# Kernel optimization log

Hardware: AMD Instinct MI355X
Metric: run time of the kernel (lower is better)

The kernel has to match this reference:

```python
import jax, jax.numpy as jnp
import numpy as np
from jax import lax

B, T, H, F, K, NB, MAXLEN = 32, 1024, 384, 384, 3, 256, 2048


def _ln(x, g, b, eps=1e-5):
    m = jnp.mean(x, axis=-1, keepdims=True)
    v = jnp.var(x, axis=-1, keepdims=True)
    return (x - m) * lax.rsqrt(v + eps) * g + b


def _conv(x, w, b):
    # x: (B, T, Cin), w: (K, Cin, Cout); SAME padding == torch padding=(K-1)//2 for K=3, stride 1
    y = lax.conv_general_dilated(x, w, (1,), 'SAME', dimension_numbers=('NWC', 'WIO', 'NWC'))
    return y + b


def _predictor(x, mask, w1, b1, g1, be1, w2, b2, g2, be2, wo, bo):
    h = _ln(jax.nn.relu(_conv(x, w1, b1)), g1, be1)
    h = _ln(jax.nn.relu(_conv(h, w2, b2)), g2, be2)
    out = jnp.einsum('btf,f->bt', h, wo) + bo  # Linear(F -> 1).squeeze(-1)
    return jnp.where(mask, 0.0, out)


def _length_regulate(x, dur, max_len):
    # vectorized equivalent of torch per-sample expand+cat+pad
    csum = jnp.cumsum(dur, axis=1)                      # (B, T)
    total = csum[:, -1]                                 # (B,) = mel_len
    frames = jnp.arange(max_len)                        # (M,)
    # frame f belongs to phoneme i with csum[i-1] <= f < csum[i]
    idx = jax.vmap(lambda c: jnp.searchsorted(c, frames, side='right'))(csum)  # (B, M)
    idx = jnp.clip(idx, 0, x.shape[1] - 1)
    out = jnp.take_along_axis(x, idx[:, :, None], axis=1)                      # (B, M, H)
    valid = (frames[None, :] < total[:, None]).astype(x.dtype)                 # zero-pad tail
    return out * valid[:, :, None], total


def setup_inputs() -> dict:
    key = jax.random.key(0)
    ks = iter(jax.random.split(key, 64))
    nk = lambda: next(ks)
    d = {}
    d['x'] = jax.random.normal(nk(), (B, T, H), jnp.float32)
    d['src_mask'] = jnp.zeros((B, T), jnp.bool_)
    d['duration'] = jax.random.randint(nk(), (B, T), 0, 4)
    d['max_len'] = MAXLEN
    for p in ('dp', 'pp', 'ep'):
        d[p + '_w1'] = jax.random.normal(nk(), (K, H, F), jnp.float32) * 0.02
        d[p + '_b1'] = jnp.zeros((F,), jnp.float32)
        d[p + '_g1'] = jnp.ones((F,), jnp.float32)
        d[p + '_be1'] = jnp.zeros((F,), jnp.float32)
        d[p + '_w2'] = jax.random.normal(nk(), (K, F, F), jnp.float32) * 0.02
        d[p + '_b2'] = jnp.zeros((F,), jnp.float32)
        d[p + '_g2'] = jnp.ones((F,), jnp.float32)
        d[p + '_be2'] = jnp.zeros((F,), jnp.float32)
        d[p + '_wo'] = jax.random.normal(nk(), (F,), jnp.float32) * 0.02
        d[p + '_bo'] = jnp.zeros((1,), jnp.float32)
    d['pitch_bins'] = jnp.linspace(0.0, 1.0, NB - 1, dtype=jnp.float32)
    d['energy_bins'] = jnp.linspace(0.0, 1.0, NB - 1, dtype=jnp.float32)
    d['pitch_emb'] = jax.random.normal(nk(), (NB, H), jnp.float32) * 0.02
    d['energy_emb'] = jax.random.normal(nk(), (NB, H), jnp.float32) * 0.02
    d['pitch_target'] = jax.random.uniform(nk(), (B, T), jnp.float32)
    d['energy_target'] = jax.random.uniform(nk(), (B, T), jnp.float32)
    return d


def reference(x, src_mask, duration, max_len,
              dp_w1, dp_b1, dp_g1, dp_be1, dp_w2, dp_b2, dp_g2, dp_be2, dp_wo, dp_bo,
              pp_w1, pp_b1, pp_g1, pp_be1, pp_w2, pp_b2, pp_g2, pp_be2, pp_wo, pp_bo,
              ep_w1, ep_b1, ep_g1, ep_be1, ep_w2, ep_b2, ep_g2, ep_be2, ep_wo, ep_bo,
              pitch_bins, energy_bins, pitch_emb, energy_emb, pitch_target, energy_target):
    log_dur = _predictor(x, src_mask, dp_w1, dp_b1, dp_g1, dp_be1, dp_w2, dp_b2, dp_g2, dp_be2, dp_wo, dp_bo)
    # phoneme-level pitch (target path: bucketize target, torch.bucketize right=False == searchsorted left)
    pitch_pred = _predictor(x, src_mask, pp_w1, pp_b1, pp_g1, pp_be1, pp_w2, pp_b2, pp_g2, pp_be2, pp_wo, pp_bo)
    x = x + pitch_emb[jnp.searchsorted(pitch_bins, pitch_target, side='left')]
    # phoneme-level energy (predictor sees x AFTER pitch embedding add, as in torch)
    energy_pred = _predictor(x, src_mask, ep_w1, ep_b1, ep_g1, ep_be1, ep_w2, ep_b2, ep_g2, ep_be2, ep_wo, ep_bo)
    x = x + energy_emb[jnp.searchsorted(energy_bins, energy_target, side='left')]
    x_out, mel_len = _length_regulate(x, duration, max_len)
    return (x_out, pitch_pred, energy_pred, log_dur, mel_len)
```

## Files before the change

### kernel.cpp

```cpp
#include <hip/hip_runtime.h>

#define B_ 32
#define T_ 1024
#define C_ 384
#define MAXLEN_ 2048
#define NBINS_ 255
#define WPK1 442368
#define ARS 392
#define AROWS 82

typedef __attribute__((ext_vector_type(8))) short short8v;
typedef __attribute__((ext_vector_type(4))) float floatx4;

__device__ __forceinline__ unsigned short f2bf(float f) {
    unsigned u = __float_as_uint(f);
    u += 0x7fffu + ((u >> 16) & 1u);
    return (unsigned short)(u >> 16);
}

struct CvP {
    const float* xf;
    const unsigned short* wpk;
    const float* b1[3];  const float* g1[3];  const float* be1[3];
    const float* b2[3];  const float* g2[3];  const float* be2[3];
    const float* wo[3];  const float* bo[3];
    float* pred[3];
    const float* pbins; const float* pemb; const float* ptgt;
};

__global__ __launch_bounds__(512, 3) void conv_fused3(CvP P)
{
    __shared__ unsigned short As[AROWS * ARS];
    float* redS  = (float*)&As[68 * ARS];
    float* redQ  = redS + 640;
    float* prbuf = redQ + 640;
    int*   embi  = (int*)(prbuf + 512);

    const int tid  = threadIdx.x;
    const int wave = tid >> 6;
    const int lane = tid & 63;
    const int lq   = lane >> 4;
    const int ln   = lane & 15;
    const int p    = blockIdx.x >> 9;
    const int bi   = blockIdx.x & 511;
    const int b    = bi >> 4;
    const int t0   = (bi & 15) << 6;
    const int nb   = wave * 48;

    const unsigned short* b1base =
        P.wpk + (size_t)p * WPK1 + (size_t)(wave * 1536) + (size_t)lane * 8;
    short8v bA[3], bB[3];
#pragma unroll
    for (int nt = 0; nt < 3; ++nt) {
        bA[nt] = *(const short8v*)(b1base + (nt << 9));
        bB[nt] = *(const short8v*)(b1base + 12288 + (nt << 9));
    }

    const bool fuse_emb = (p == 2);
    if (fuse_emb) {
        if (tid < 68) {
            const int t = t0 - 2 + tid;
            int lo = 0;
            if ((unsigned)t < (unsigned)T_) {
                const float tg = P.ptgt[(b << 10) + t];
                int hi = NBINS_;
                while (lo < hi) {
                    const int mid = (lo + hi) >> 1;
                    if (P.pbins[mid] < tg) lo = mid + 1; else hi = mid;
                }
            }
            embi[tid] = lo;
        }
        __syncthreads();
    }
    for (int i = tid; i < 68 * 96; i += 512) {
        const int row = i / 96;
        const int c4  = i - row * 96;
        const int t   = t0 - 2 + row;
        uint2 pv = make_uint2(0u, 0u);
        if ((unsigned)t < (unsigned)T_) {
            float4 f = *(const float4*)(P.xf + ((size_t)(b << 10) + t) * C_ + c4 * 4);
            if (fuse_emb) {
                const float* er = P.pemb + (size_t)embi[row] * C_ + c4 * 4;
                f.x += er[0]; f.y += er[1]; f.z += er[2]; f.w += er[3];
            }
            asm("v_cvt_pk_bf16_f32 %0, %1, %2" : "=v"(pv.x) : "v"(f.x), "v"(f.y));
            asm("v_cvt_pk_bf16_f32 %0, %1, %2" : "=v"(pv.y) : "v"(f.z), "v"(f.w));
        }
        *(uint2*)&As[row * ARS + c4 * 4] = pv;
    }
    __syncthreads();

    floatx4 acc1[15];
#pragma unroll
    for (int i = 0; i < 15; ++i) acc1[i] = (floatx4){0.f, 0.f, 0.f, 0.f};

    const unsigned short* abase = &As[ln * ARS + lq * 8];
    {
        const unsigned short* bpA = b1base + 2 * 12288;
        const unsigned short* bpB = b1base + 3 * 12288;
#pragma unroll
        for (int kc = 0; kc < 3; ++kc) {
#pragma unroll
            for (int h2 = 0; h2 < 6; ++h2) {
                const int hb = h2 * 64;
                const int r  = kc * 12 + h2 * 2;
                {
                    short8v afrag[5];
#pragma unroll
                    for (int mt = 0; mt < 5; ++mt)
                        afrag[mt] = *(const short8v*)(abase + (mt * 16 + kc) * ARS + hb);
#pragma unroll
                    for (int mt = 0; mt < 5; ++mt)
#pragma unroll
                        for (int nt = 0; nt < 3; ++nt)
                            acc1[mt * 3 + nt] = __builtin_amdgcn_mfma_f32_16x16x32_bf16(
                                afrag[mt], bA[nt], acc1[mt * 3 + nt], 0, 0, 0);
                    if (r + 2 < 36) {
#pragma unroll
                        for (int nt = 0; nt < 3; ++nt)
                            bA[nt] = *(const short8v*)(bpA + (nt << 9));
                        bpA += 24576;
                    }
                }
                {
                    short8v afrag[5];
#pragma unroll
                    for (int mt = 0; mt < 5; ++mt)
                        afrag[mt] = *(const short8v*)(abase + (mt * 16 + kc) * ARS + hb + 32);
#pragma unroll
                    for (int mt = 0; mt < 5; ++mt)
#pragma unroll
                        for (int nt = 0; nt < 3; ++nt)
                            acc1[mt * 3 + nt] = __builtin_amdgcn_mfma_f32_16x16x32_bf16(
                                afrag[mt], bB[nt], acc1[mt * 3 + nt], 0, 0, 0);
                    if (r + 3 < 36) {
#pragma unroll
                        for (int nt = 0; nt < 3; ++nt)
                            bB[nt] = *(const short8v*)(bpB + (nt << 9));
                        bpB += 24576;
                    }
                }
            }
        }
    }
    __syncthreads();

    float c1b[3], c1g[3], c1be[3];
#pragma unroll
    for (int nt = 0; nt < 3; ++nt) {
        const int col = nb + nt * 16 + ln;
        c1b[nt]  = P.b1[p][col];
        c1g[nt]  = P.g1[p][col];
        c1be[nt] = P.be1[p][col];
    }
#pragma unroll
    for (int mt = 0; mt < 5; ++mt) {
#pragma unroll
        for (int rg = 0; rg < 4; ++rg) {
            float s = 0.f, q = 0.f;
#pragma unroll
            for (int nt = 0; nt < 3; ++nt) {
                float v = acc1[mt * 3 + nt][rg] + c1b[nt];
                v = v > 0.f ? v : 0.f;
                acc1[mt * 3 + nt][rg] = v;
                s += v; q += v * v;
            }
#pragma unroll
            for (int off = 1; off < 16; off <<= 1) {
                s += __shfl_xor(s, off, 64);
                q += __shfl_xor(q, off, 64);
            }
            if (ln == ((mt * 4 + rg) & 15)) {
                redS[wave * 80 + mt * 16 + lq * 4 + rg] = s;
                redQ[wave * 80 + mt * 16 + lq * 4 + rg] = q;
            }
        }
    }
    __syncthreads();

#pragma unroll
    for (int mt = 0; mt < 5; ++mt) {
#pragma unroll
        for (int rg = 0; rg < 4; ++rg) {
            const int j = mt * 16 + lq * 4 + rg;
            if (j < 66) {
                const int th = t0 - 1 + j;
                float s = 0.f, q = 0.f;
#pragma unroll
                for (int w = 0; w < 8; ++w) {
                    s += redS[w * 80 + j];
                    q += redQ[w * 80 + j];
                }
                const float m  = s * (1.f / 384.f);
                const float rs = rsqrtf(q * (1.f / 384.f) - m * m + 1e-5f);
                const bool valid = (unsigned)th < (unsigned)T_;
#pragma unroll
                for (int nt = 0; nt < 3; ++nt) {
                    float v = (acc1[mt * 3 + nt][rg] - m) * rs * c1g[nt] + c1be[nt];
                    if (!valid) v = 0.f;
                    As[j * ARS + nb + nt * 16 + ln] = f2bf(v);
                }
            }
        }
    }

    const unsigned short* b2base =
        P.wpk + (size_t)(3 + p) * WPK1 + (size_t)(wave * 1536) + (size_t)lane * 8;
#pragma unroll
    for (int nt = 0; nt < 3; ++nt) {
        bA[nt] = *(const short8v*)(b2base + (nt << 9));
        bB[nt] = *(const short8v*)(b2base + 12288 + (nt << 9));
    }
    __syncthreads();

    floatx4 acc2[12];
#pragma unroll
    for (int i = 0; i < 12; ++i) acc2[i] = (floatx4){0.f, 0.f, 0.f, 0.f};
    {
        const unsigned short* bpA = b2base + 2 * 12288;
        const unsigned short* bpB = b2base + 3 * 12288;
#pragma unroll
        for (int kc = 0; kc < 3; ++kc) {
#pragma unroll
            for (int h2 = 0; h2 < 6; ++h2) {
                const int hb = h2 * 64;
                const int r  = kc * 12 + h2 * 2;
                {
                    short8v afrag[4];
#pragma unroll
                    for (int mt = 0; mt < 4; ++mt)
                        afrag[mt] = *(const short8v*)(abase + (mt * 16 + kc) * ARS + hb);
#pragma unroll
                    for (int mt = 0; mt < 4; ++mt)
#pragma unroll
                        for (int nt = 0; nt < 3; ++nt)
                            acc2[mt * 3 + nt] = __builtin_amdgcn_mfma_f32_16x16x32_bf16(
                                afrag[mt], bA[nt], acc2[mt * 3 + nt], 0, 0, 0);
                    if (r + 2 < 36) {
#pragma unroll
                        for (int nt = 0; nt < 3; ++nt)
                            bA[nt] = *(const short8v*)(bpA + (nt << 9));
                        bpA += 24576;
                    }
                }
                {
                    short8v afrag[4];
#pragma unroll
                    for (int mt = 0; mt < 4; ++mt)
                        afrag[mt] = *(const short8v*)(abase + (mt * 16 + kc) * ARS + hb + 32);
#pragma unroll
                    for (int mt = 0; mt < 4; ++mt)
#pragma unroll
                        for (int nt = 0; nt < 3; ++nt)
                            acc2[mt * 3 + nt] = __builtin_amdgcn_mfma_f32_16x16x32_bf16(
                                afrag[mt], bB[nt], acc2[mt * 3 + nt], 0, 0, 0);
                    if (r + 3 < 36) {
#pragma unroll
                        for (int nt = 0; nt < 3; ++nt)
                            bB[nt] = *(const short8v*)(bpB + (nt << 9));
                        bpB += 24576;
                    }
                }
            }
        }
    }

    float c2b[3], c2g[3], c2be[3], cwo[3];
#pragma unroll
    for (int nt = 0; nt < 3; ++nt) {
        const int col = nb + nt * 16 + ln;
        c2b[nt]  = P.b2[p][col];
        c2g[nt]  = P.g2[p][col];
        c2be[nt] = P.be2[p][col];
        cwo[nt]  = P.wo[p][col];
    }
#pragma unroll
    for (int mt = 0; mt < 4; ++mt) {
#pragma unroll
        for (int rg = 0; rg < 4; ++rg) {
            float s = 0.f, q = 0.f;
#pragma unroll
            for (int nt = 0; nt < 3; ++nt) {
                float v = acc2[mt * 3 + nt][rg] + c2b[nt];
                v = v > 0.f ? v : 0.f;
                acc2[mt * 3 + nt][rg] = v;
                s += v; q += v * v;
            }
#pragma unroll
            for (int off = 1; off < 16; off <<= 1) {
                s += __shfl_xor(s, off, 64);
                q += __shfl_xor(q, off, 64);
            }
            if (ln == ((mt * 4 + rg) & 15)) {
                redS[wave * 80 + mt * 16 + lq * 4 + rg] = s;
                redQ[wave * 80 + mt * 16 + lq * 4 + rg] = q;
            }
        }
    }
    __syncthreads();

#pragma unroll
    for (int mt = 0; mt < 4; ++mt) {
#pragma unroll
        for (int rg = 0; rg < 4; ++rg) {
            const int row = mt * 16 + lq * 4 + rg;
            float s = 0.f, q = 0.f;
#pragma unroll
            for (int w = 0; w < 8; ++w) {
                s += redS[w * 80 + row];
                q += redQ[w * 80 + row];
            }
            const float m  = s * (1.f / 384.f);
            const float rs = rsqrtf(q * (1.f / 384.f) - m * m + 1e-5f);
            float pr = 0.f;
#pragma unroll
            for (int nt = 0; nt < 3; ++nt)
                pr += ((acc2[mt * 3 + nt][rg] - m) * rs * c2g[nt] + c2be[nt]) * cwo[nt];
#pragma unroll
            for (int off = 1; off < 16; off <<= 1)
                pr += __shfl_xor(pr, off, 64);
            if (ln == ((mt * 4 + rg) & 15))
                prbuf[wave * 64 + row] = pr;
        }
    }
    __syncthreads();
    if (tid < 64) {
        float s = P.bo[p][0];
#pragma unroll
        for (int w = 0; w < 8; ++w) s += prbuf[w * 64 + tid];
        P.pred[p][(bi << 6) + tid] = s;
    }
}

#define WSS 388
__global__ __launch_bounds__(256) void pack_w_kernel(
    const float* __restrict__ s0, const float* __restrict__ s1,
    const float* __restrict__ s2, const float* __restrict__ s3,
    const float* __restrict__ s4, const float* __restrict__ s5,
    unsigned short* __restrict__ dst)
{
    __shared__ float ws[32 * WSS];
    const int blk  = blockIdx.x;
    const int wsel = blk / 36;
    const int r    = blk - wsel * 36;
    const float* src = wsel == 0 ? s0 : wsel == 1 ? s1 : wsel == 2 ? s2
                     : wsel == 3 ? s3 : wsel == 4 ? s4 : s5;
    const int tid = threadIdx.x;

    const float* sb = src + (size_t)r * 32 * C_;
    for (int i4 = tid; i4 < 3072; i4 += 256) {
        const int k  = i4 / 96;
        const int n4 = i4 - k * 96;
        *(float4*)&ws[k * WSS + n4 * 4] = *(const float4*)(sb + (size_t)k * C_ + n4 * 4);
    }
    __syncthreads();

    unsigned short* db = dst + (size_t)wsel * WPK1 + (size_t)r * 12288;
    for (int c = tid; c < 1536; c += 256) {
        const int lane = c & 63;
        const int wnt  = c >> 6;
        const int ln   = lane & 15;
        const int lq   = lane >> 4;
        const int n    = wnt * 16 + ln;
        ushort4 o0, o1;
        unsigned short e[8];
#pragma unroll
        for (int j = 0; j < 8; ++j)
            e[j] = f2bf(ws[(lq * 8 + j) * WSS + n]);
        o0 = make_ushort4(e[0], e[1], e[2], e[3]);
        o1 = make_ushort4(e[4], e[5], e[6], e[7]);
        *(ushort4*)(db + wnt * 512 + lane * 8)     = o0;
        *(ushort4*)(db + wnt * 512 + lane * 8 + 4) = o1;
    }
}

__global__ __launch_bounds__(256) void cumsum_idx_kernel(
    const int* __restrict__ dur,
    const float* __restrict__ pbins, const float* __restrict__ ptgt,
    const float* __restrict__ ebins, const float* __restrict__ etgt,
    int* __restrict__ xidx, float* __restrict__ mel_len)
{
    __shared__ int cs[T_];
    __shared__ int part[256];
    __shared__ float pb[NBINS_], eb[NBINS_];
    const int b = blockIdx.x;
    const int tid = threadIdx.x;
    if (tid < NBINS_) { pb[tid] = pbins[tid]; eb[tid] = ebins[tid]; }
    int l[4];
    int s = 0;
#pragma unroll
    for (int i = 0; i < 4; ++i) { l[i] = dur[(b << 10) + tid * 4 + i]; s += l[i]; }
    part[tid] = s;
    __syncthreads();
    for (int off = 1; off < 256; off <<= 1) {
        int u = 0;
        if (tid >= off) u = part[tid - off];
        __syncthreads();
        part[tid] += u;
        __syncthreads();
    }
    const int incl = part[tid];
    int run = incl - s;
#pragma unroll
    for (int i = 0; i < 4; ++i) {
        run += l[i];
        cs[tid * 4 + i] = run;
    }
    if (tid == 255) mel_len[b] = (float)incl;
    __syncthreads();
    const int total = cs[T_ - 1];
    for (int f = tid; f < MAXLEN_; f += 256) {
        int pk = -1;
        if (f < total) {
            int lo = 0, hi = T_;
            while (lo < hi) {
                const int mid = (lo + hi) >> 1;
                if (cs[mid] <= f) lo = mid + 1; else hi = mid;
            }
            const int t = lo > T_ - 1 ? T_ - 1 : lo;
            const int row = (b << 10) + t;
            const float ptg = ptgt[row];
            int plo = 0, phi = NBINS_;
            while (plo < phi) {
                const int mid = (plo + phi) >> 1;
                if (pb[mid] < ptg) plo = mid + 1; else phi = mid;
            }
            const float etg = etgt[row];
            int elo = 0, ehi = NBINS_;
            while (elo < ehi) {
                const int mid = (elo + ehi) >> 1;
                if (eb[mid] < etg) elo = mid + 1; else ehi = mid;
            }
            pk = t | (plo << 10) | (elo << 19);
        }
        xidx[(b << 11) + f] = pk;
    }
}

__global__ __launch_bounds__(256) void length_reg_kernel(
    const float* __restrict__ x, const int* __restrict__ xidx,
    const float* __restrict__ pemb, const float* __restrict__ eemb,
    float* __restrict__ out)
{
    const int g    = blockIdx.x * 256 + threadIdx.x;
    const int c4   = g % 96;
    const int rest = g / 96;
    const int frame = rest & (MAXLEN_ - 1);
    const int b     = rest >> 11;
    const int pk = xidx[(b << 11) + frame];
    float4 v = make_float4(0.f, 0.f, 0.f, 0.f);
    if (pk >= 0) {
        const int t   = pk & 1023;
        const int plo = (pk >> 10) & 511;
        const int elo = (pk >> 19) & 511;
        v = *(const float4*)(x + ((size_t)(b << 10) + t) * C_ + c4 * 4);
        const float4 pe = *(const float4*)(pemb + (size_t)plo * C_ + c4 * 4);
        const float4 ee = *(const float4*)(eemb + (size_t)elo * C_ + c4 * 4);
        v.x += pe.x + ee.x; v.y += pe.y + ee.y;
        v.z += pe.z + ee.z; v.w += pe.w + ee.w;
    }
    *(float4*)(out + (size_t)g * 4) = v;
}

extern "C" void kernel_launch(void* const* d_in, const int* in_sizes, int n_in,
                              void* d_out, int out_size, void* d_ws, size_t ws_size,
                              hipStream_t stream)
{
    const float* x        = (const float*)d_in[0];
    const int*   duration = (const int*)d_in[2];
    const float* P[3][10];
    for (int p = 0; p < 3; ++p)
        for (int q = 0; q < 10; ++q)
            P[p][q] = (const float*)d_in[4 + p * 10 + q];
    const float* pitch_bins    = (const float*)d_in[34];
    const float* energy_bins   = (const float*)d_in[35];
    const float* pitch_emb     = (const float*)d_in[36];
    const float* energy_emb    = (const float*)d_in[37];
    const float* pitch_target  = (const float*)d_in[38];
    const float* energy_target = (const float*)d_in[39];

    float* out_x      = (float*)d_out;
    float* out_pitch  = out_x + (size_t)B_ * MAXLEN_ * C_;
    float* out_energy = out_pitch + B_ * T_;
    float* out_logdur = out_energy + B_ * T_;
    float* out_mellen = out_logdur + B_ * T_;

    unsigned short* wpk = (unsigned short*)d_ws;
    int* xidx = (int*)(wpk + (size_t)6 * WPK1);

    const dim3 blk(256);
    const dim3 cblk(512);

    pack_w_kernel<<<216, blk, 0, stream>>>(
        P[0][0], P[0][4], P[1][0], P[1][4], P[2][0], P[2][4], wpk);

    CvP Pa;
    Pa.xf = x; Pa.wpk = wpk;
    for (int p = 0; p < 3; ++p) {
        Pa.b1[p]  = P[p][1];
        Pa.g1[p]  = P[p][2];
        Pa.be1[p] = P[p][3];
        Pa.b2[p]  = P[p][5];
        Pa.g2[p]  = P[p][6];
        Pa.be2[p] = P[p][7];
        Pa.wo[p]  = P[p][8];
        Pa.bo[p]  = P[p][9];
    }
    Pa.pred[0] = out_logdur; Pa.pred[1] = out_pitch; Pa.pred[2] = out_energy;
    Pa.pbins = pitch_bins; Pa.pemb = pitch_emb; Pa.ptgt = pitch_target;

    conv_fused3<<<1536, cblk, 0, stream>>>(Pa);

    cumsum_idx_kernel<<<B_, blk, 0, stream>>>(
        duration, pitch_bins, pitch_target, energy_bins, energy_target,
        xidx, out_mellen);
    length_reg_kernel<<<24576, blk, 0, stream>>>(
        x, xidx, pitch_emb, energy_emb, out_x);
}
```

Measured before the change: 522.4 us.

## Retile fused conv to 62-row outputs so first conv uses four M-tiles

Changes the time tiling of the fused two-conv predictor kernel from 64 output rows per block to 62, so the halo for the first conv fits in 64 rows (4 MFMA M-tiles instead of 5). This cuts the wasted first-layer MFMA work and the LDS footprint. The cost is more blocks (17 tiles per sequence instead of 16), a partial last tile, and about 3% more total output rows recomputed at halos. It also makes weight base pointers wave-uniform with readfirstlane, so they can sit in scalar registers.

```diff
diff --git a/kernel.cpp b/kernel.cpp
--- a/kernel.cpp
+++ b/kernel.cpp
@@ -7,7 +7,8 @@
 #define NBINS_ 255
 #define WPK1 442368
 #define ARS 392
-#define AROWS 82
+#define TROWS 62
+#define NTILE 17
 
 typedef __attribute__((ext_vector_type(8))) short short8v;
 typedef __attribute__((ext_vector_type(4))) float floatx4;
@@ -16,6 +17,13 @@
     unsigned u = __float_as_uint(f);
     u += 0x7fffu + ((u >> 16) & 1u);
     return (unsigned short)(u >> 16);
+}
+
+__device__ __forceinline__ const unsigned short* rfl(const unsigned short* p) {
+    unsigned long long u = (unsigned long long)p;
+    unsigned lo = __builtin_amdgcn_readfirstlane((unsigned)u);
+    unsigned hi = __builtin_amdgcn_readfirstlane((unsigned)(u >> 32));
+    return (const unsigned short*)(((unsigned long long)hi << 32) | lo);
 }
 
 struct CvP {
@@ -30,35 +38,37 @@
 
 __global__ __launch_bounds__(512, 3) void conv_fused3(CvP P)
 {
-    __shared__ unsigned short As[AROWS * ARS];
-    float* redS  = (float*)&As[68 * ARS];
-    float* redQ  = redS + 640;
-    float* prbuf = redQ + 640;
-    int*   embi  = (int*)(prbuf + 512);
+    __shared__ unsigned short As[66 * ARS];
+    __shared__ float redS[8 * 64];
+    __shared__ float redQ[8 * 64];
+    __shared__ float prbuf[512];
+    __shared__ int embi[66];
 
     const int tid  = threadIdx.x;
     const int wave = tid >> 6;
     const int lane = tid & 63;
     const int lq   = lane >> 4;
     const int ln   = lane & 15;
-    const int p    = blockIdx.x >> 9;
-    const int bi   = blockIdx.x & 511;
-    const int b    = bi >> 4;
-    const int t0   = (bi & 15) << 6;
+    const int blk  = blockIdx.x;
+    const int p    = blk / (B_ * NTILE);
+    const int rem  = blk - p * (B_ * NTILE);
+    const int b    = rem / NTILE;
+    const int k    = rem - b * NTILE;
+    const int t0   = k * TROWS;
     const int nb   = wave * 48;
 
-    const unsigned short* b1base =
-        P.wpk + (size_t)p * WPK1 + (size_t)(wave * 1536) + (size_t)lane * 8;
+    const unsigned short* b1s = rfl(P.wpk + (size_t)p * WPK1 + wave * 1536);
+    const int lo8 = lane * 8;
     short8v bA[3], bB[3];
 #pragma unroll
     for (int nt = 0; nt < 3; ++nt) {
-        bA[nt] = *(const short8v*)(b1base + (nt << 9));
-        bB[nt] = *(const short8v*)(b1base + 12288 + (nt << 9));
+        bA[nt] = *(const short8v*)(b1s + lo8 + (nt << 9));
+        bB[nt] = *(const short8v*)(b1s + lo8 + 12288 + (nt << 9));
     }
 
     const bool fuse_emb = (p == 2);
     if (fuse_emb) {
-        if (tid < 68) {
+        if (tid < 66) {
             const int t = t0 - 2 + tid;
             int lo = 0;
             if ((unsigned)t < (unsigned)T_) {
@@ -73,7 +83,7 @@
         }
         __syncthreads();
     }
-    for (int i = tid; i < 68 * 96; i += 512) {
+    for (int i = tid; i < 66 * 96; i += 512) {
         const int row = i / 96;
         const int c4  = i - row * 96;
         const int t   = t0 - 2 + row;
@@ -91,14 +101,14 @@
     }
     __syncthreads();
 
-    floatx4 acc1[15];
-#pragma unroll
-    for (int i = 0; i < 15; ++i) acc1[i] = (floatx4){0.f, 0.f, 0.f, 0.f};
+    floatx4 acc1[12];
+#pragma unroll
+    for (int i = 0; i < 12; ++i) acc1[i] = (floatx4){0.f, 0.f, 0.f, 0.f};
 
     const unsigned short* abase = &As[ln * ARS + lq * 8];
     {
-        const unsigned short* bpA = b1base + 2 * 12288;
-        const unsigned short* bpB = b1base + 3 * 12288;
+        int offA = lo8 + 2 * 12288;
+        int offB = lo8 + 3 * 12288;
 #pragma unroll
         for (int kc = 0; kc < 3; ++kc) {
 #pragma unroll
@@ -106,12 +116,12 @@
                 const int hb = h2 * 64;
                 const int r  = kc * 12 + h2 * 2;
                 {
-                    short8v afrag[5];
-#pragma unroll
-                    for (int mt = 0; mt < 5; ++mt)
+                    short8v afrag[4];
+#pragma unroll
+                    for (int mt = 0; mt < 4; ++mt)
                         afrag[mt] = *(const short8v*)(abase + (mt * 16 + kc) * ARS + hb);
 #pragma unroll
-                    for (int mt = 0; mt < 5; ++mt)
+                    for (int mt = 0; mt < 4; ++mt)
 #pragma unroll
                         for (int nt = 0; nt < 3; ++nt)
                             acc1[mt * 3 + nt] = __builtin_amdgcn_mfma_f32_16x16x32_bf16(
@@ -119,17 +129,17 @@
                     if (r + 2 < 36) {
 #pragma unroll
                         for (int nt = 0; nt < 3; ++nt)
-                            bA[nt] = *(const short8v*)(bpA + (nt << 9));
-                        bpA += 24576;
+                            bA[nt] = *(const short8v*)(b1s + offA + (nt << 9));
+                        offA += 24576;
                     }
                 }
                 {
-                    short8v afrag[5];
-#pragma unroll
-                    for (int mt = 0; mt < 5; ++mt)
+                    short8v afrag[4];
+#pragma unroll
+                    for (int mt = 0; mt < 4; ++mt)
                         afrag[mt] = *(const short8v*)(abase + (mt * 16 + kc) * ARS + hb + 32);
 #pragma unroll
-                    for (int mt = 0; mt < 5; ++mt)
+                    for (int mt = 0; mt < 4; ++mt)
 #pragma unroll
                         for (int nt = 0; nt < 3; ++nt)
                             acc1[mt * 3 + nt] = __builtin_amdgcn_mfma_f32_16x16x32_bf16(
@@ -137,8 +147,8 @@
                     if (r + 3 < 36) {
 #pragma unroll
                         for (int nt = 0; nt < 3; ++nt)
-                            bB[nt] = *(const short8v*)(bpB + (nt << 9));
-                        bpB += 24576;
+                            bB[nt] = *(const short8v*)(b1s + offB + (nt << 9));
+                        offB += 24576;
                     }
                 }
             }
@@ -155,7 +165,7 @@
         c1be[nt] = P.be1[p][col];
     }
 #pragma unroll
-    for (int mt = 0; mt < 5; ++mt) {
+    for (int mt = 0; mt < 4; ++mt) {
 #pragma unroll
         for (int rg = 0; rg < 4; ++rg) {
             float s = 0.f, q = 0.f;
@@ -172,45 +182,42 @@
                 q += __shfl_xor(q, off, 64);
             }
             if (ln == ((mt * 4 + rg) & 15)) {
-                redS[wave * 80 + mt * 16 + lq * 4 + rg] = s;
-                redQ[wave * 80 + mt * 16 + lq * 4 + rg] = q;
-            }
-        }
-    }
-    __syncthreads();
-
-#pragma unroll
-    for (int mt = 0; mt < 5; ++mt) {
+                redS[wave * 64 + mt * 16 + lq * 4 + rg] = s;
+                redQ[wave * 64 + mt * 16 + lq * 4 + rg] = q;
+            }
+        }
+    }
+    __syncthreads();
+
+#pragma unroll
+    for (int mt = 0; mt < 4; ++mt) {
 #pragma unroll
         for (int rg = 0; rg < 4; ++rg) {
-            const int j = mt * 16 + lq * 4 + rg;
-            if (j < 66) {
-                const int th = t0 - 1 + j;
-                float s = 0.f, q = 0.f;
-#pragma unroll
-                for (int w = 0; w < 8; ++w) {
-                    s += redS[w * 80 + j];
-                    q += redQ[w * 80 + j];
-                }
-                const float m  = s * (1.f / 384.f);
-                const float rs = rsqrtf(q * (1.f / 384.f) - m * m + 1e-5f);
-                const bool valid = (unsigned)th < (unsigned)T_;
-#pragma unroll
-                for (int nt = 0; nt < 3; ++nt) {
-                    float v = (acc1[mt * 3 + nt][rg] - m) * rs * c1g[nt] + c1be[nt];
-                    if (!valid) v = 0.f;
-                    As[j * ARS + nb + nt * 16 + ln] = f2bf(v);
-                }
-            }
-        }
-    }
-
-    const unsigned short* b2base =
-        P.wpk + (size_t)(3 + p) * WPK1 + (size_t)(wave * 1536) + (size_t)lane * 8;
+            const int j  = mt * 16 + lq * 4 + rg;
+            const int th = t0 - 1 + j;
+            float s = 0.f, q = 0.f;
+#pragma unroll
+            for (int w = 0; w < 8; ++w) {
+                s += redS[w * 64 + j];
+                q += redQ[w * 64 + j];
+            }
+            const float m  = s * (1.f / 384.f);
+            const float rs = rsqrtf(q * (1.f / 384.f) - m * m + 1e-5f);
+            const bool valid = (unsigned)th < (unsigned)T_;
+#pragma unroll
+            for (int nt = 0; nt < 3; ++nt) {
+                float v = (acc1[mt * 3 + nt][rg] - m) * rs * c1g[nt] + c1be[nt];
+                if (!valid) v = 0.f;
+                As[j * ARS + nb + nt * 16 + ln] = f2bf(v);
+            }
+        }
+    }
+
+    const unsigned short* b2s = rfl(P.wpk + (size_t)(3 + p) * WPK1 + wave * 1536);
 #pragma unroll
     for (int nt = 0; nt < 3; ++nt) {
-        bA[nt] = *(const short8v*)(b2base + (nt << 9));
-        bB[nt] = *(const short8v*)(b2base + 12288 + (nt << 9));
+        bA[nt] = *(const short8v*)(b2s + lo8 + (nt << 9));
+        bB[nt] = *(const short8v*)(b2s + lo8 + 12288 + (nt << 9));
     }
     __syncthreads();
 
@@ -218,8 +225,8 @@
 #pragma unroll
     for (int i = 0; i < 12; ++i) acc2[i] = (floatx4){0.f, 0.f, 0.f, 0.f};
     {
-        const unsigned short* bpA = b2base + 2 * 12288;
-        const unsigned short* bpB = b2base + 3 * 12288;
+        int offA = lo8 + 2 * 12288;
+        int offB = lo8 + 3 * 12288;
 #pragma unroll
         for (int kc = 0; kc < 3; ++kc) {
 #pragma unroll
@@ -240,8 +247,8 @@
                     if (r + 2 < 36) {
 #pragma unroll
                         for (int nt = 0; nt < 3; ++nt)
-                            bA[nt] = *(const short8v*)(bpA + (nt << 9));
-                        bpA += 24576;
+                            bA[nt] = *(const short8v*)(b2s + offA + (nt << 9));
+                        offA += 24576;
                     }
                 }
                 {
@@ -258,8 +265,8 @@
                     if (r + 3 < 36) {
 #pragma unroll
                         for (int nt = 0; nt < 3; ++nt)
-                            bB[nt] = *(const short8v*)(bpB + (nt << 9));
-                        bpB += 24576;
+                            bB[nt] = *(const short8v*)(b2s + offB + (nt << 9));
+                        offB += 24576;
                     }
                 }
             }
@@ -293,8 +300,8 @@
                 q += __shfl_xor(q, off, 64);
             }
             if (ln == ((mt * 4 + rg) & 15)) {
-                redS[wave * 80 + mt * 16 + lq * 4 + rg] = s;
-                redQ[wave * 80 + mt * 16 + lq * 4 + rg] = q;
+                redS[wave * 64 + mt * 16 + lq * 4 + rg] = s;
+                redQ[wave * 64 + mt * 16 + lq * 4 + rg] = q;
             }
         }
     }
@@ -308,8 +315,8 @@
             float s = 0.f, q = 0.f;
 #pragma unroll
             for (int w = 0; w < 8; ++w) {
-                s += redS[w * 80 + row];
-                q += redQ[w * 80 + row];
+                s += redS[w * 64 + row];
+                q += redQ[w * 64 + row];
             }
             const float m  = s * (1.f / 384.f);
             const float rs = rsqrtf(q * (1.f / 384.f) - m * m + 1e-5f);
@@ -326,10 +333,13 @@
     }
     __syncthreads();
     if (tid < 64) {
-        float s = P.bo[p][0];
-#pragma unroll
-        for (int w = 0; w < 8; ++w) s += prbuf[w * 64 + tid];
-        P.pred[p][(bi << 6) + tid] = s;
+        const int t = t0 + tid;
+        if (tid < TROWS && t < T_) {
+            float s = P.bo[p][0];
+#pragma unroll
+            for (int w = 0; w < 8; ++w) s += prbuf[w * 64 + tid];
+            P.pred[p][(b << 10) + t] = s;
+        }
     }
 }
 
@@ -510,7 +520,7 @@
     Pa.pred[0] = out_logdur; Pa.pred[1] = out_pitch; Pa.pred[2] = out_energy;
     Pa.pbins = pitch_bins; Pa.pemb = pitch_emb; Pa.ptgt = pitch_target;
 
-    conv_fused3<<<1536, cblk, 0, stream>>>(Pa);
+    conv_fused3<<<3 * B_ * NTILE, cblk, 0, stream>>>(Pa);
 
     cumsum_idx_kernel<<<B_, blk, 0, stream>>>(
         duration, pitch_bins, pitch_target, energy_bins, energy_target,
```

New measurement: 569.0 us. +8.9%, slower.
